# Kernel tuning notes

Hardware: AMD Instinct MI355X
Metric: run time of the kernel (lower is better)

The kernel has to match this reference:

```python
import jax, jax.numpy as jnp
import numpy as np

D_K = 64  # from init_kwargs

def setup_inputs() -> dict:
    key = jax.random.key(0)
    k1, k2, k3 = jax.random.split(key, 3)
    B, H, S = 2, 16, 2048
    q = jax.random.normal(k1, (B, H, S, D_K), dtype=jnp.float32)
    k = jax.random.normal(k2, (B, H, D_K, S), dtype=jnp.float32)
    v = jax.random.normal(k3, (B, H, S, D_K), dtype=jnp.float32)
    return {"q": q, "k": k, "v": v}

def reference(q, k, v):
    # scores = q @ k / sqrt(d_k)  -> [B,H,S,S]; k is pre-transposed [B,H,d_k,S]
    scale = 1.0 / (D_K ** 0.5)
    scores = jnp.einsum('bhsd,bhdt->bhst', q, k) * scale
    attn = jax.nn.softmax(scores, axis=-1)
    context = jnp.einsum('bhst,bhtd->bhsd', attn, v)
    return (context, attn)
```

## Files before the change

### kernel.cpp

```cpp
#include <hip/hip_runtime.h>

typedef __attribute__((ext_vector_type(4))) float    f32x4;
typedef __attribute__((ext_vector_type(8))) short    short8;
typedef __attribute__((ext_vector_type(4))) unsigned uint4v;

#define BH_   32
#define S_    2048
#define DK_   64
#define TQ_   128
#define NT_   256
#define C_    64
#define NCH_  (S_ / C_)
#define NBLK_ (BH_ * (S_ / TQ_))
#define SCALE_LOG2E 0.18033688011112042f

#define QP_ELEMS (BH_ * 128 * 64 * 16)
#define KP_ELEMS (BH_ * NCH_ * 8 * 64 * 8)
#define VP_ELEMS KP_ELEMS
#define WS_NEEDED ((size_t)(QP_ELEMS + KP_ELEMS + VP_ELEMS) * 2)

#define PROW_  68
#define PPLANE_ (16 * PROW_)

__device__ __forceinline__ unsigned short f2bf(float x) {
    unsigned u = __builtin_bit_cast(unsigned, x);
    u += 0x7FFFu + ((u >> 16) & 1u);
    return (unsigned short)(u >> 16);
}
__device__ __forceinline__ float e2(float x) { return __builtin_amdgcn_exp2f(x); }

__global__ __launch_bounds__(256)
void sdpa_prepack_kernel(const float* __restrict__ q, const float* __restrict__ k,
                         const float* __restrict__ v, unsigned short* __restrict__ qp,
                         unsigned short* __restrict__ kp, unsigned short* __restrict__ vp)
{
    const int bid = blockIdx.x;
    const int tid = threadIdx.x;
    if (bid < 2048) {
        const int i  = bid * 256 + tid;
        const int sl = i & 63, s = (i >> 6) & 7, ch = (i >> 9) & 31, bh = i >> 14;
        const int sg = sl >> 4, sn = sl & 15;
        const float* base = k + (size_t)bh * DK_ * S_
                              + (size_t)(32 * (s & 1) + 8 * sg) * S_
                              + ch * C_ + 16 * (s >> 1) + sn;
        short8 t;
#pragma unroll
        for (int j = 0; j < 8; ++j) t[j] = (short)f2bf(base[(size_t)j * S_]);
        *(short8*)&kp[(size_t)i * 8] = t;
    } else if (bid < 4096) {
        const int i  = (bid - 2048) * 256 + tid;
        const int sl = i & 63, s = (i >> 6) & 7, ch = (i >> 9) & 31, bh = i >> 14;
        const int sg = sl >> 4, sn = sl & 15;
        const float* base = v + (size_t)bh * S_ * DK_
                              + (size_t)(ch * C_ + 32 * (s & 1) + 4 * sg) * DK_
                              + 16 * (s >> 1) + sn;
        short8 t;
#pragma unroll
        for (int j = 0; j < 4; ++j) {
            t[j]     = (short)f2bf(base[(size_t)j * DK_]);
            t[4 + j] = (short)f2bf(base[(size_t)(16 + j) * DK_]);
        }
        *(short8*)&vp[(size_t)i * 8] = t;
    } else {
        const int i  = (bid - 4096) * 256 + tid;
        const int l  = i & 63, tg = (i >> 6) & 127, bh = i >> 13;
        const int g  = l >> 4, ln = l & 15;
        const float* qr = q + ((size_t)bh * S_ + tg * 16 + ln) * DK_;
        short8 t0, t1;
#pragma unroll
        for (int j = 0; j < 8; ++j) {
            t0[j] = (short)f2bf(qr[8 * g + j]      * SCALE_LOG2E);
            t1[j] = (short)f2bf(qr[32 + 8 * g + j] * SCALE_LOG2E);
        }
        *(short8*)&qp[(size_t)i * 16]     = t0;
        *(short8*)&qp[(size_t)i * 16 + 8] = t1;
    }
}

__global__ __launch_bounds__(NT_)
void sdpa_main_kernel(const unsigned short* __restrict__ qp,
                      const unsigned short* __restrict__ kp,
                      const unsigned short* __restrict__ vp,
                      float* __restrict__ ctx, float* __restrict__ attn)
{
    __shared__ float plds[4 * 2 * PPLANE_];

    const int tid = threadIdx.x;
    const int w   = tid >> 6;
    const int l   = tid & 63;
    const int g   = l >> 4;
    const int ln  = l & 15;

    float* pl = &plds[w * 2 * PPLANE_];

    const int orig = blockIdx.x;
    const int bid  = (orig & 7) * 64 + (orig >> 3);

    const int bh   = bid >> 4;
    const int qb   = bid & 15;
    const int row0 = qb * TQ_;

    const unsigned short* kph = kp + (size_t)bh * (NCH_ * 8 * 64 * 8) + (size_t)l * 8;
    const unsigned short* vph = vp + (size_t)bh * (NCH_ * 8 * 64 * 8) + (size_t)l * 8;

    short8 aq[2][2];
#pragma unroll
    for (int rt = 0; rt < 2; ++rt) {
        const size_t qi = ((size_t)(bh * 128 + qb * 8 + w * 2 + rt) * 64 + l) * 16;
        aq[rt][0] = *(const short8*)&qp[qi];
        aq[rt][1] = *(const short8*)&qp[qi + 8];
    }

    float lsum[2] = {0.f, 0.f};
    short8 kfA[8], kfB[8];
#pragma unroll
    for (int s = 0; s < 8; ++s)
        kfA[s] = *(const short8*)(kph + (size_t)s * 512);

#define SUM_STEP(KF)                                                            \
    _Pragma("unroll")                                                           \
    for (int ct = 0; ct < 4; ++ct) {                                            \
        _Pragma("unroll")                                                       \
        for (int rt = 0; rt < 2; ++rt) {                                        \
            f32x4 acc = {0.f, 0.f, 0.f, 0.f};                                   \
            acc = __builtin_amdgcn_mfma_f32_16x16x32_bf16(KF[2*ct],   aq[rt][0], acc, 0, 0, 0); \
            acc = __builtin_amdgcn_mfma_f32_16x16x32_bf16(KF[2*ct+1], aq[rt][1], acc, 0, 0, 0); \
            lsum[rt] += (e2(acc[0]) + e2(acc[1])) + (e2(acc[2]) + e2(acc[3]));  \
        }                                                                       \
    }

    for (int ch = 0; ch < NCH_; ch += 2) {
#pragma unroll
        for (int s = 0; s < 8; ++s)
            kfB[s] = *(const short8*)(kph + ((size_t)(ch + 1) * 8 + s) * 512);
        SUM_STEP(kfA)
        if (ch + 2 < NCH_) {
#pragma unroll
            for (int s = 0; s < 8; ++s)
                kfA[s] = *(const short8*)(kph + ((size_t)(ch + 2) * 8 + s) * 512);
        }
        SUM_STEP(kfB)
    }
#undef SUM_STEP

    float lrec[2];
#pragma unroll
    for (int rt = 0; rt < 2; ++rt) {
        float t = lsum[rt];
        t += __shfl_xor(t, 16);
        t += __shfl_xor(t, 32);
        lrec[rt] = 1.0f / t;
    }

    f32x4 cacc[2][4];
#pragma unroll
    for (int rt = 0; rt < 2; ++rt)
#pragma unroll
        for (int dt = 0; dt < 4; ++dt) cacc[rt][dt] = (f32x4){0.f, 0.f, 0.f, 0.f};

    float* attwb = attn + ((size_t)bh * S_ + row0 + w * 32 + (l >> 4)) * S_ + (l & 15) * 4;

#pragma unroll
    for (int s = 0; s < 8; ++s)
        kfA[s] = *(const short8*)(kph + (size_t)s * 512);

#define EMIT_STEP(CH, KF, VF)                                                   \
    {                                                                           \
        const int c0 = (CH) * C_;                                               \
        unsigned pau[2][2][4];                                                  \
        _Pragma("unroll")                                                       \
        for (int ct = 0; ct < 4; ++ct) {                                        \
            const int kb2 = ct >> 1, hf = ct & 1;                               \
            _Pragma("unroll")                                                   \
            for (int rt = 0; rt < 2; ++rt) {                                    \
                f32x4 acc = {0.f, 0.f, 0.f, 0.f};                               \
                acc = __builtin_amdgcn_mfma_f32_16x16x32_bf16(KF[2*ct],   aq[rt][0], acc, 0, 0, 0); \
                acc = __builtin_amdgcn_mfma_f32_16x16x32_bf16(KF[2*ct+1], aq[rt][1], acc, 0, 0, 0); \
                f32x4 p;                                                        \
                _Pragma("unroll")                                               \
                for (int r = 0; r < 4; ++r) p[r] = e2(acc[r]) * lrec[rt];       \
                *(f32x4*)&pl[rt * PPLANE_ + ln * PROW_ + 16 * ct + 4 * g] = p;  \
                pau[rt][kb2][hf * 2 + 0] = (unsigned)f2bf(p[0]) | ((unsigned)f2bf(p[1]) << 16); \
                pau[rt][kb2][hf * 2 + 1] = (unsigned)f2bf(p[2]) | ((unsigned)f2bf(p[3]) << 16); \
            }                                                                   \
        }                                                                       \
        _Pragma("unroll")                                                       \
        for (int kb2 = 0; kb2 < 2; ++kb2) {                                     \
            _Pragma("unroll")                                                   \
            for (int rt = 0; rt < 2; ++rt) {                                    \
                uint4v pw = {pau[rt][kb2][0], pau[rt][kb2][1], pau[rt][kb2][2], pau[rt][kb2][3]}; \
                const short8 pa = __builtin_bit_cast(short8, pw);               \
                _Pragma("unroll")                                               \
                for (int dt = 0; dt < 4; ++dt)                                  \
                    cacc[rt][dt] = __builtin_amdgcn_mfma_f32_16x16x32_bf16(pa, VF[dt * 2 + kb2], cacc[rt][dt], 0, 0, 0); \
            }                                                                   \
        }                                                                       \
             \
        _Pragma("unroll")                                                       \
        for (int rt = 0; rt < 2; ++rt) {                                        \
            _Pragma("unroll")                                                   \
            for (int u = 0; u < 4; ++u) {                                       \
                const f32x4 pr = *(const f32x4*)&pl[rt * PPLANE_                \
                                     + (4 * u + (l >> 4)) * PROW_ + 4 * (l & 15)]; \
                __builtin_nontemporal_store(pr,                                 \
                    (f32x4*)(attwb + (size_t)(rt * 16 + 4 * u) * S_ + c0));     \
            }                                                                   \
        }                                                                       \
    }

    for (int ch = 0; ch < NCH_; ch += 2) {
        short8 vfA[8];
#pragma unroll
        for (int s = 0; s < 8; ++s)
            vfA[s] = *(const short8*)(vph + ((size_t)ch * 8 + s) * 512);
#pragma unroll
        for (int s = 0; s < 8; ++s)
            kfB[s] = *(const short8*)(kph + ((size_t)(ch + 1) * 8 + s) * 512);
        EMIT_STEP(ch, kfA, vfA)

        short8 vfB[8];
#pragma unroll
        for (int s = 0; s < 8; ++s)
            vfB[s] = *(const short8*)(vph + ((size_t)(ch + 1) * 8 + s) * 512);
        if (ch + 2 < NCH_) {
#pragma unroll
            for (int s = 0; s < 8; ++s)
                kfA[s] = *(const short8*)(kph + ((size_t)(ch + 2) * 8 + s) * 512);
        }
        EMIT_STEP(ch + 1, kfB, vfB)
    }
#undef EMIT_STEP

#pragma unroll
    for (int rt = 0; rt < 2; ++rt) {
        float* cw = ctx + ((size_t)bh * S_ + row0 + w * 32 + rt * 16 + 4 * g) * DK_ + ln;
#pragma unroll
        for (int dt = 0; dt < 4; ++dt)
#pragma unroll
            for (int r = 0; r < 4; ++r)
                __builtin_nontemporal_store(cacc[rt][dt][r], cw + (size_t)r * DK_ + 16 * dt);
    }
}

__global__ __launch_bounds__(NT_, 4)
void sdpa_fallback_kernel(const float* __restrict__ q, const float* __restrict__ k,
                          const float* __restrict__ v, float* __restrict__ ctx,
                          float* __restrict__ attn)
{
    __shared__ unsigned short klds[8 * 64 * 8];
    __shared__ unsigned short vlds[8 * 64 * 8];

    const int tid = threadIdx.x;
    const int w   = tid >> 6;
    const int l   = tid & 63;
    const int g   = l >> 4;
    const int ln  = l & 15;

    const int bh   = blockIdx.x >> 5;
    const int qb   = blockIdx.x & 31;
    const int row0 = qb * 64;

    const float* kb = k + (size_t)bh * DK_ * S_;
    const float* vb = v + (size_t)bh * S_ * DK_;

    const int s0 = tid >> 6;
    const int sl = tid & 63;
    const int sg = sl >> 4, sn = sl & 15;

    const float* kg0 = kb + (size_t)(32 * (s0 & 1) + 8 * sg) * S_ + 16 * (s0 >> 1) + sn;
    const float* kg1 = kb + (size_t)(32 * (s0 & 1) + 8 * sg) * S_ + 16 * ((s0 + 4) >> 1) + sn;
    const float* vg0 = vb + (size_t)(32 * (s0 & 1) + 4 * sg) * DK_ + 16 * (s0 >> 1) + sn;
    const float* vg1 = vb + (size_t)(32 * (s0 & 1) + 4 * sg) * DK_ + 16 * ((s0 + 4) >> 1) + sn;

    unsigned short* kw0 = &klds[((s0    ) * 64 + sl) * 8];
    unsigned short* kw1 = &klds[((s0 + 4) * 64 + sl) * 8];
    unsigned short* vw0 = &vlds[((s0    ) * 64 + sl) * 8];
    unsigned short* vw1 = &vlds[((s0 + 4) * 64 + sl) * 8];

    auto stageK = [&](const float* base, unsigned short* dst, int c0) {
        short8 t;
#pragma unroll
        for (int j = 0; j < 8; ++j)
            t[j] = (short)f2bf(base[(size_t)j * S_ + c0]);
        *(short8*)dst = t;
    };
    auto stageV = [&](const float* base, unsigned short* dst, int t0) {
        short8 t;
#pragma unroll
        for (int j = 0; j < 4; ++j) {
            t[j]     = (short)f2bf(base[(size_t)(t0 + j) * DK_]);
            t[4 + j] = (short)f2bf(base[(size_t)(t0 + 16 + j) * DK_]);
        }
        *(short8*)dst = t;
    };

    const float* qrow = q + ((size_t)bh * S_ + row0 + w * 16 + ln) * DK_;
    short8 aq0, aq1;
#pragma unroll
    for (int j = 0; j < 8; ++j) {
        aq0[j] = (short)f2bf(qrow[g * 8 + j]      * SCALE_LOG2E);
        aq1[j] = (short)f2bf(qrow[g * 8 + 32 + j] * SCALE_LOG2E);
    }

    float lsum = 0.f;
    for (int ch = 0; ch < NCH_; ++ch) {
        const int c0 = ch * C_;
        __syncthreads();
        stageK(kg0, kw0, c0);
        stageK(kg1, kw1, c0);
        __syncthreads();
#pragma unroll
        for (int ct = 0; ct < 4; ++ct) {
            const short8 kf0 = *(const short8*)&klds[((ct * 2 + 0) * 64 + l) * 8];
            const short8 kf1 = *(const short8*)&klds[((ct * 2 + 1) * 64 + l) * 8];
            f32x4 acc = {0.f, 0.f, 0.f, 0.f};
            acc = __builtin_amdgcn_mfma_f32_16x16x32_bf16(kf0, aq0, acc, 0, 0, 0);
            acc = __builtin_amdgcn_mfma_f32_16x16x32_bf16(kf1, aq1, acc, 0, 0, 0);
            lsum += (e2(acc[0]) + e2(acc[1])) + (e2(acc[2]) + e2(acc[3]));
        }
    }
    lsum += __shfl_xor(lsum, 16);
    lsum += __shfl_xor(lsum, 32);
    const float lrec = 1.0f / lsum;

    f32x4 cacc[4];
#pragma unroll
    for (int dt = 0; dt < 4; ++dt) cacc[dt] = (f32x4){0.f, 0.f, 0.f, 0.f};

    float* attw = attn + ((size_t)bh * S_ + row0 + w * 16 + ln) * S_ + 4 * g;

    for (int ch = 0; ch < NCH_; ++ch) {
        const int c0 = ch * C_;
        __syncthreads();
        stageK(kg0, kw0, c0);
        stageK(kg1, kw1, c0);
        stageV(vg0, vw0, c0);
        stageV(vg1, vw1, c0);
        __syncthreads();

        unsigned pau[2][4];
#pragma unroll
        for (int ct = 0; ct < 4; ++ct) {
            const short8 kf0 = *(const short8*)&klds[((ct * 2 + 0) * 64 + l) * 8];
            const short8 kf1 = *(const short8*)&klds[((ct * 2 + 1) * 64 + l) * 8];
            f32x4 acc = {0.f, 0.f, 0.f, 0.f};
            acc = __builtin_amdgcn_mfma_f32_16x16x32_bf16(kf0, aq0, acc, 0, 0, 0);
            acc = __builtin_amdgcn_mfma_f32_16x16x32_bf16(kf1, aq1, acc, 0, 0, 0);

            f32x4 p;
#pragma unroll
            for (int r = 0; r < 4; ++r) p[r] = e2(acc[r]) * lrec;
            *(f32x4*)(attw + c0 + 16 * ct) = p;

            const int kb2 = ct >> 1, hf = ct & 1;
            pau[kb2][hf * 2 + 0] = (unsigned)f2bf(p[0]) | ((unsigned)f2bf(p[1]) << 16);
            pau[kb2][hf * 2 + 1] = (unsigned)f2bf(p[2]) | ((unsigned)f2bf(p[3]) << 16);
        }

#pragma unroll
        for (int kb2 = 0; kb2 < 2; ++kb2) {
            uint4v pw = {pau[kb2][0], pau[kb2][1], pau[kb2][2], pau[kb2][3]};
            const short8 pa = __builtin_bit_cast(short8, pw);
#pragma unroll
            for (int dt = 0; dt < 4; ++dt) {
                const short8 vf = *(const short8*)&vlds[((dt * 2 + kb2) * 64 + l) * 8];
                cacc[dt] = __builtin_amdgcn_mfma_f32_16x16x32_bf16(pa, vf, cacc[dt], 0, 0, 0);
            }
        }
    }

    float* cw = ctx + ((size_t)bh * S_ + row0 + w * 16 + 4 * g) * DK_ + ln;
#pragma unroll
    for (int dt = 0; dt < 4; ++dt)
#pragma unroll
        for (int r = 0; r < 4; ++r)
            cw[(size_t)r * DK_ + 16 * dt] = cacc[dt][r];
}

extern "C" void kernel_launch(void* const* d_in, const int* in_sizes, int n_in,
                              void* d_out, int out_size, void* d_ws, size_t ws_size,
                              hipStream_t stream)
{
    const float* q = (const float*)d_in[0];
    const float* k = (const float*)d_in[1];
    const float* v = (const float*)d_in[2];
    float* ctx  = (float*)d_out;
    float* attn = (float*)d_out + (size_t)BH_ * S_ * DK_;

    if (ws_size >= WS_NEEDED) {
        unsigned short* qp = (unsigned short*)d_ws;
        unsigned short* kp = qp + QP_ELEMS;
        unsigned short* vp = kp + KP_ELEMS;
        sdpa_prepack_kernel<<<dim3(5120), dim3(256), 0, stream>>>(q, k, v, qp, kp, vp);
        sdpa_main_kernel<<<dim3(NBLK_), dim3(NT_), 0, stream>>>(qp, kp, vp, ctx, attn);
    } else {
        sdpa_fallback_kernel<<<dim3(BH_ * 32), dim3(NT_), 0, stream>>>(q, k, v, ctx, attn);
    }
}
```

Baseline: 161.6 us.

## Split softmax row-sum pass into separate kernel with wave-split key chunks

```diff
diff --git a/kernel.cpp b/kernel.cpp
--- a/kernel.cpp
+++ b/kernel.cpp
@@ -17,7 +17,8 @@
 #define QP_ELEMS (BH_ * 128 * 64 * 16)
 #define KP_ELEMS (BH_ * NCH_ * 8 * 64 * 8)
 #define VP_ELEMS KP_ELEMS
-#define WS_NEEDED ((size_t)(QP_ELEMS + KP_ELEMS + VP_ELEMS) * 2)
+#define LREC_ELEMS (BH_ * S_)
+#define WS_NEEDED ((size_t)(QP_ELEMS + KP_ELEMS + VP_ELEMS) * 2 + (size_t)LREC_ELEMS * 4)
 
 #define PROW_  68
 #define PPLANE_ (16 * PROW_)
@@ -77,13 +78,12 @@
     }
 }
 
-__global__ __launch_bounds__(NT_)
-void sdpa_main_kernel(const unsigned short* __restrict__ qp,
+__global__ __launch_bounds__(256, 4)
+void sdpa_sums_kernel(const unsigned short* __restrict__ qp,
                       const unsigned short* __restrict__ kp,
-                      const unsigned short* __restrict__ vp,
-                      float* __restrict__ ctx, float* __restrict__ attn)
+                      float* __restrict__ lrecb)
 {
-    __shared__ float plds[4 * 2 * PPLANE_];
+    __shared__ float red[4][4][16];
 
     const int tid = threadIdx.x;
     const int w   = tid >> 6;
@@ -91,6 +91,69 @@
     const int g   = l >> 4;
     const int ln  = l & 15;
 
+    const int orig = blockIdx.x;
+    const int bid  = (orig & 7) * 128 + (orig >> 3);
+
+    const int bh   = bid >> 5;
+    const int qt   = bid & 31;
+    const int row0 = qt * 64;
+
+    const unsigned short* kph = kp + (size_t)bh * (NCH_ * 8 * 64 * 8) + (size_t)l * 8;
+
+    short8 aq[4][2];
+#pragma unroll
+    for (int rt = 0; rt < 4; ++rt) {
+        const size_t qi = ((size_t)(bh * 128 + qt * 4 + rt) * 64 + l) * 16;
+        aq[rt][0] = *(const short8*)&qp[qi];
+        aq[rt][1] = *(const short8*)&qp[qi + 8];
+    }
+
+    float lsum[4] = {0.f, 0.f, 0.f, 0.f};
+    for (int ch = w; ch < NCH_; ch += 4) {
+        short8 kf[8];
+#pragma unroll
+        for (int s = 0; s < 8; ++s)
+            kf[s] = *(const short8*)(kph + ((size_t)ch * 8 + s) * 512);
+#pragma unroll
+        for (int ct = 0; ct < 4; ++ct) {
+#pragma unroll
+            for (int rt = 0; rt < 4; ++rt) {
+                f32x4 acc = {0.f, 0.f, 0.f, 0.f};
+                acc = __builtin_amdgcn_mfma_f32_16x16x32_bf16(kf[2 * ct],     aq[rt][0], acc, 0, 0, 0);
+                acc = __builtin_amdgcn_mfma_f32_16x16x32_bf16(kf[2 * ct + 1], aq[rt][1], acc, 0, 0, 0);
+                lsum[rt] += (e2(acc[0]) + e2(acc[1])) + (e2(acc[2]) + e2(acc[3]));
+            }
+        }
+    }
+#pragma unroll
+    for (int rt = 0; rt < 4; ++rt) {
+        float t = lsum[rt];
+        t += __shfl_xor(t, 16);
+        t += __shfl_xor(t, 32);
+        if (g == 0) red[w][rt][ln] = t;
+    }
+    __syncthreads();
+    if (w == 0) {
+        const float total = (red[0][g][ln] + red[1][g][ln]) + (red[2][g][ln] + red[3][g][ln]);
+        lrecb[(size_t)bh * S_ + row0 + g * 16 + ln] = 1.0f / total;
+    }
+}
+
+__global__ __launch_bounds__(NT_)
+void sdpa_emit_kernel(const unsigned short* __restrict__ qp,
+                      const unsigned short* __restrict__ kp,
+                      const unsigned short* __restrict__ vp,
+                      const float* __restrict__ lrecb,
+                      float* __restrict__ ctx, float* __restrict__ attn)
+{
+    __shared__ float plds[4 * 2 * PPLANE_];
+
+    const int tid = threadIdx.x;
+    const int w   = tid >> 6;
+    const int l   = tid & 63;
+    const int g   = l >> 4;
+    const int ln  = l & 15;
+
     float* pl = &plds[w * 2 * PPLANE_];
 
     const int orig = blockIdx.x;
@@ -104,62 +167,24 @@
     const unsigned short* vph = vp + (size_t)bh * (NCH_ * 8 * 64 * 8) + (size_t)l * 8;
 
     short8 aq[2][2];
+    float  lrec[2];
 #pragma unroll
     for (int rt = 0; rt < 2; ++rt) {
         const size_t qi = ((size_t)(bh * 128 + qb * 8 + w * 2 + rt) * 64 + l) * 16;
         aq[rt][0] = *(const short8*)&qp[qi];
         aq[rt][1] = *(const short8*)&qp[qi + 8];
-    }
-
-    float lsum[2] = {0.f, 0.f};
+        lrec[rt]  = lrecb[(size_t)bh * S_ + row0 + w * 32 + rt * 16 + ln];
+    }
+
+    f32x4 cacc[2][4];
+#pragma unroll
+    for (int rt = 0; rt < 2; ++rt)
+#pragma unroll
+        for (int dt = 0; dt < 4; ++dt) cacc[rt][dt] = (f32x4){0.f, 0.f, 0.f, 0.f};
+
+    float* attwb = attn + ((size_t)bh * S_ + row0 + w * 32 + (l >> 4)) * S_ + (l & 15) * 4;
+
     short8 kfA[8], kfB[8];
-#pragma unroll
-    for (int s = 0; s < 8; ++s)
-        kfA[s] = *(const short8*)(kph + (size_t)s * 512);
-
-#define SUM_STEP(KF)                                                            \
-    _Pragma("unroll")                                                           \
-    for (int ct = 0; ct < 4; ++ct) {                                            \
-        _Pragma("unroll")                                                       \
-        for (int rt = 0; rt < 2; ++rt) {                                        \
-            f32x4 acc = {0.f, 0.f, 0.f, 0.f};                                   \
-            acc = __builtin_amdgcn_mfma_f32_16x16x32_bf16(KF[2*ct],   aq[rt][0], acc, 0, 0, 0); \
-            acc = __builtin_amdgcn_mfma_f32_16x16x32_bf16(KF[2*ct+1], aq[rt][1], acc, 0, 0, 0); \
-            lsum[rt] += (e2(acc[0]) + e2(acc[1])) + (e2(acc[2]) + e2(acc[3]));  \
-        }                                                                       \
-    }
-
-    for (int ch = 0; ch < NCH_; ch += 2) {
-#pragma unroll
-        for (int s = 0; s < 8; ++s)
-            kfB[s] = *(const short8*)(kph + ((size_t)(ch + 1) * 8 + s) * 512);
-        SUM_STEP(kfA)
-        if (ch + 2 < NCH_) {
-#pragma unroll
-            for (int s = 0; s < 8; ++s)
-                kfA[s] = *(const short8*)(kph + ((size_t)(ch + 2) * 8 + s) * 512);
-        }
-        SUM_STEP(kfB)
-    }
-#undef SUM_STEP
-
-    float lrec[2];
-#pragma unroll
-    for (int rt = 0; rt < 2; ++rt) {
-        float t = lsum[rt];
-        t += __shfl_xor(t, 16);
-        t += __shfl_xor(t, 32);
-        lrec[rt] = 1.0f / t;
-    }
-
-    f32x4 cacc[2][4];
-#pragma unroll
-    for (int rt = 0; rt < 2; ++rt)
-#pragma unroll
-        for (int dt = 0; dt < 4; ++dt) cacc[rt][dt] = (f32x4){0.f, 0.f, 0.f, 0.f};
-
-    float* attwb = attn + ((size_t)bh * S_ + row0 + w * 32 + (l >> 4)) * S_ + (l & 15) * 4;
-
 #pragma unroll
     for (int s = 0; s < 8; ++s)
         kfA[s] = *(const short8*)(kph + (size_t)s * 512);
@@ -388,11 +413,13 @@
     float* attn = (float*)d_out + (size_t)BH_ * S_ * DK_;
 
     if (ws_size >= WS_NEEDED) {
-        unsigned short* qp = (unsigned short*)d_ws;
-        unsigned short* kp = qp + QP_ELEMS;
-        unsigned short* vp = kp + KP_ELEMS;
+        unsigned short* qp   = (unsigned short*)d_ws;
+        unsigned short* kp   = qp + QP_ELEMS;
+        unsigned short* vp   = kp + KP_ELEMS;
+        float*          lrec = (float*)(vp + VP_ELEMS);
         sdpa_prepack_kernel<<<dim3(5120), dim3(256), 0, stream>>>(q, k, v, qp, kp, vp);
-        sdpa_main_kernel<<<dim3(NBLK_), dim3(NT_), 0, stream>>>(qp, kp, vp, ctx, attn);
+        sdpa_sums_kernel<<<dim3(1024), dim3(256), 0, stream>>>(qp, kp, lrec);
+        sdpa_emit_kernel<<<dim3(NBLK_), dim3(NT_), 0, stream>>>(qp, kp, vp, lrec, ctx, attn);
     } else {
         sdpa_fallback_kernel<<<dim3(BH_ * 32), dim3(NT_), 0, stream>>>(q, k, v, ctx, attn);
     }
```

Result: slower. 178.9 us (+10.7%).
